# Kernel tuning notes

Measured on AMD Instinct MI355X. Metric: run time of the kernel, lower is better.

Reference implementation:

```python
import jax, jax.numpy as jnp
import numpy as np

KS = 3          # kernel_size
NH = 6          # num_heads
NUM_TOK = KS ** 3  # 27 neighbors per query


def setup_inputs() -> dict:
    key = jax.random.key(0)
    k1, k2, k3 = jax.random.split(key, 3)
    q = jax.random.normal(k1, (1, 40, 40, 40, 96), dtype=jnp.float32)
    k = jax.random.normal(k2, (1, 40, 40, 40, 96), dtype=jnp.float32)
    rpb = jax.random.normal(k3, (NH, KS, KS, KS), dtype=jnp.float32) * 0.02
    return {"q": q, "k": k, "rpb": rpb}


def _offsets():
    # torch.arange(-3//2+1, 3//2+1) == arange(-1, 2); meshgrid 'ij'; stacked -> [27, 3]
    r = jnp.arange(-1, 2, dtype=jnp.float32)
    g = jnp.stack(jnp.meshgrid(r, r, r, indexing="ij"), axis=-1)
    return g.reshape(NUM_TOK, 3)


def reference(q, k, rpb):
    B, H, W, T, C = q.shape
    hd = C // NH
    scale = hd ** -0.5
    N = H * W * T

    # queries: [B, N, nh, hd], pre-scaled
    qh = q.reshape(B, N, NH, hd) * scale

    # zero-pad keys by 1 voxel on each spatial side (matches nnf.pad on channels-first k)
    kp = jnp.pad(jnp.transpose(k, (0, 4, 1, 2, 3)),
                 ((0, 0), (0, 0), (1, 1), (1, 1), (1, 1)))

    # 27 shifted views == torch unfold over a 3x3x3 window (i slowest, matches grid order)
    wins = [kp[:, :, i:i + H, j:j + W, l:l + T]
            for i in range(KS) for j in range(KS) for l in range(KS)]
    Kw = jnp.stack(wins, axis=2)                 # [B, C, 27, H, W, T]
    Kw = Kw.reshape(B, NH, hd, NUM_TOK, N)        # [B, nh, hd, 27, N]

    # attention logits over the 27-token neighborhood
    attn = jnp.einsum("bnhd,bhdkn->bnhk", qh, Kw)  # [B, N, nh, 27]
    attn = attn + rpb.reshape(NH, NUM_TOK)[None, None, :, :]  # relative position bias
    attn = jax.nn.softmax(attn, axis=-1)

    # expected displacement: weighted sum of integer offsets -> [B, N, nh, 3]
    x = jnp.einsum("bnhk,kc->bnhc", attn, _offsets())
    x = x.reshape(B, H, W, T, NH * 3)
    return jnp.transpose(x, (0, 4, 1, 2, 3))      # [B, nh*3, H, W, T]
```

## Files before the change

### kernel.cpp

```cpp
#include <hip/hip_runtime.h>

typedef _Float16 hh2 __attribute__((ext_vector_type(2)));

#define DH 40
#define DW 40
#define DT 40
#define NC 96
#define NH 6
#define HD 16
#define NTOK 27
#define NVOX (DH * DW * DT)

#define TX 8
#define TY 4
#define TZ 8
#define HX 10
#define HY 6
#define HZ 10
#define NHALO 600

#define TXN 5
#define TYN 10
#define TZN 5
#define NTILE 250
#define NJOB 1500
#define NXCD 8
#define GRID 1504
#define PER_XCD (GRID / NXCD)

__device__ __forceinline__ float dot2acc(hh2 a, hh2 b, float c) {
    return __builtin_amdgcn_fdot2(a, b, c, false);
}
__device__ __forceinline__ hh2 pkrtz(float a, float b) {
    return __builtin_bit_cast(hh2, __builtin_amdgcn_cvt_pkrtz(a, b));
}
__device__ __forceinline__ unsigned int pkbits(float a, float b) {
    return __builtin_bit_cast(unsigned int, __builtin_amdgcn_cvt_pkrtz(a, b));
}

union I4H {
    int4 v[2];
    hh2 h[8];
};

__global__ __launch_bounds__(256) void natt_disp_kernel(
    const float* __restrict__ q,
    const float* __restrict__ k,
    const float* __restrict__ rpb,
    float* __restrict__ out)
{
    __shared__ int4 s_k[NHALO * 2];

    const int job = (blockIdx.x & (NXCD - 1)) * PER_XCD + (blockIdx.x >> 3);
    if (job >= NJOB) return;

    const int h    = job % NH;
    const int tile = job / NH;
    const int tz = tile % TZN;
    const int ty = (tile / TZN) % TYN;
    const int tx = tile / (TZN * TYN);
    const int x0 = tx * TX, y0 = ty * TY, z0 = tz * TZ;

    const int tid = threadIdx.x;

    float rk[NTOK];
    {
        const float* rb = rpb + h * NTOK;
        #pragma unroll
        for (int kk = 0; kk < NTOK; ++kk) rk[kk] = rb[kk];
    }

    const float* kh = k + h * HD;

    #pragma unroll
    for (int it = 0; it < 10; ++it) {
        const int jj = tid + it * 256;
        if (jj < NHALO * 4) {
            const int n = jj >> 2;
            const int c = jj & 3;
            const int hx = n / (HY * HZ);
            const int r  = n - hx * (HY * HZ);
            const int hy = r / HZ;
            const int hz = r - hy * HZ;
            const int gx = x0 - 1 + hx;
            const int gy = y0 - 1 + hy;
            const int gz = z0 - 1 + hz;
            uint2 w; w.x = 0u; w.y = 0u;
            if (((unsigned)gx < DH) & ((unsigned)gy < DW) & ((unsigned)gz < DT)) {
                const float4 a = *(const float4*)(
                    kh + ((size_t)((gx * DW + gy) * DT + gz)) * NC + c * 4);
                w.x = pkbits(a.x, a.y);
                w.y = pkbits(a.z, a.w);
            }
            const int p = hy & 1;
            ((uint2*)s_k)[((n * 2 + (c >> 1)) ^ p) * 2 + (c & 1)] = w;
        }
    }

    const int lz = tid & (TZ - 1);
    const int ly = (tid >> 3) & (TY - 1);
    const int lx = tid >> 5;
    const int vox = ((x0 + lx) * DW + (y0 + ly)) * DT + (z0 + lz);

    hh2 qh[8];
    {
        const float4* qv = (const float4*)(q + (size_t)vox * NC + h * HD);
        const float4 a = qv[0], b = qv[1], c = qv[2], d = qv[3];
        qh[0] = pkrtz(a.x, a.y);
        qh[1] = pkrtz(a.z, a.w);
        qh[2] = pkrtz(b.x, b.y);
        qh[3] = pkrtz(b.z, b.w);
        qh[4] = pkrtz(c.x, c.y);
        qh[5] = pkrtz(c.z, c.w);
        qh[6] = pkrtz(d.x, d.y);
        qh[7] = pkrtz(d.z, d.w);
    }

    __syncthreads();

    float l[NTOK];
    #pragma unroll
    for (int i = 0; i < 3; ++i) {
        #pragma unroll
        for (int j = 0; j < 3; ++j) {
            const int base = ((lx + i) * HY + (ly + j)) * HZ + lz;
            const int p = (ly + j) & 1;
            #pragma unroll
            for (int ll = 0; ll < 3; ++ll) {
                const int n = base + ll;
                I4H u;
                u.v[0] = s_k[(n * 2 + 0) ^ p];
                u.v[1] = s_k[(n * 2 + 1) ^ p];
                float d = 0.0f;
                d = dot2acc(qh[0], u.h[0], d);
                d = dot2acc(qh[1], u.h[1], d);
                d = dot2acc(qh[2], u.h[2], d);
                d = dot2acc(qh[3], u.h[3], d);
                d = dot2acc(qh[4], u.h[4], d);
                d = dot2acc(qh[5], u.h[5], d);
                d = dot2acc(qh[6], u.h[6], d);
                d = dot2acc(qh[7], u.h[7], d);
                const int kk = (i * 3 + j) * 3 + ll;
                l[kk] = fmaf(d, 0.25f, rk[kk]);
            }
        }
    }

    float g0 = fmaxf(fmaxf(l[0],  l[1]),  l[2]);
    float g1 = fmaxf(fmaxf(l[3],  l[4]),  l[5]);
    float g2 = fmaxf(fmaxf(l[6],  l[7]),  l[8]);
    float g3 = fmaxf(fmaxf(l[9],  l[10]), l[11]);
    float g4 = fmaxf(fmaxf(l[12], l[13]), l[14]);
    float g5 = fmaxf(fmaxf(l[15], l[16]), l[17]);
    float g6 = fmaxf(fmaxf(l[18], l[19]), l[20]);
    float g7 = fmaxf(fmaxf(l[21], l[22]), l[23]);
    float g8 = fmaxf(fmaxf(l[24], l[25]), l[26]);
    float t0 = fmaxf(fmaxf(g0, g1), g2);
    float t1 = fmaxf(fmaxf(g3, g4), g5);
    float t2 = fmaxf(fmaxf(g6, g7), g8);
    const float m = fmaxf(fmaxf(t0, t1), t2);

    const float LOG2E = 1.44269504f;
    const float nm2 = -m * LOG2E;
    float e[NTOK];
    #pragma unroll
    for (int kk = 0; kk < NTOK; ++kk)
        e[kk] = exp2f(fmaf(l[kk], LOG2E, nm2));

    float s[9], zp[9];
    #pragma unroll
    for (int g = 0; g < 9; ++g) {
        s[g]  = (e[g * 3] + e[g * 3 + 1]) + e[g * 3 + 2];
        zp[g] = e[g * 3 + 2] - e[g * 3];
    }
    const float sum = ((s[0] + s[1]) + (s[2] + s[3]))
                    + ((s[4] + s[5]) + (s[6] + s[7])) + s[8];
    const float szs = ((zp[0] + zp[1]) + (zp[2] + zp[3]))
                    + ((zp[4] + zp[5]) + (zp[6] + zp[7])) + zp[8];
    const float sxs = ((s[6] + s[7]) + s[8]) - ((s[0] + s[1]) + s[2]);
    const float sys = ((s[2] + s[5]) + s[8]) - ((s[0] + s[3]) + s[6]);

    const float inv = __builtin_amdgcn_rcpf(sum);

    out[((size_t)(h * 3 + 0)) * NVOX + vox] = sxs * inv;
    out[((size_t)(h * 3 + 1)) * NVOX + vox] = sys * inv;
    out[((size_t)(h * 3 + 2)) * NVOX + vox] = szs * inv;
}

extern "C" void kernel_launch(void* const* d_in, const int* in_sizes, int n_in,
                              void* d_out, int out_size, void* d_ws, size_t ws_size,
                              hipStream_t stream) {
    const float* q   = (const float*)d_in[0];
    const float* k   = (const float*)d_in[1];
    const float* rpb = (const float*)d_in[2];
    float* out = (float*)d_out;

    natt_disp_kernel<<<GRID, 256, 0, stream>>>(q, k, rpb, out);
}
```

Measured before the change: 20.92 us.

## Process two heads per block with register-prefetched second head and max-free softmax

Each block now handles two heads instead of one, halving the grid. The second head's K halo and Q are loaded into registers while the first head computes from shared memory, then staged into a second LDS buffer. The softmax drops the max subtraction and accumulates exp2 values directly, with the scale and log2e folded into the constants. This trades higher register pressure (launch bounds 256,3) and a risk of overflow on unbounded logits for fewer blocks and overlap of load latency with compute.

```diff
diff --git a/kernel.cpp b/kernel.cpp
--- a/kernel.cpp
+++ b/kernel.cpp
@@ -19,23 +19,19 @@
 #define HZ 10
 #define NHALO 600
 
-#define TXN 5
-#define TYN 10
-#define TZN 5
 #define NTILE 250
-#define NJOB 1500
-#define NXCD 8
-#define GRID 1504
-#define PER_XCD (GRID / NXCD)
+#define NBLK 750
+#define GRID 752
+#define PER_XCD 94
 
 __device__ __forceinline__ float dot2acc(hh2 a, hh2 b, float c) {
     return __builtin_amdgcn_fdot2(a, b, c, false);
 }
-__device__ __forceinline__ hh2 pkrtz(float a, float b) {
-    return __builtin_bit_cast(hh2, __builtin_amdgcn_cvt_pkrtz(a, b));
-}
 __device__ __forceinline__ unsigned int pkbits(float a, float b) {
     return __builtin_bit_cast(unsigned int, __builtin_amdgcn_cvt_pkrtz(a, b));
+}
+__device__ __forceinline__ hh2 asz(unsigned int u) {
+    return __builtin_bit_cast(hh2, u);
 }
 
 union I4H {
@@ -43,34 +39,44 @@
     hh2 h[8];
 };
 
-__global__ __launch_bounds__(256) void natt_disp_kernel(
+__global__ __launch_bounds__(256, 3) void natt_disp_kernel(
     const float* __restrict__ q,
     const float* __restrict__ k,
     const float* __restrict__ rpb,
     float* __restrict__ out)
 {
-    __shared__ int4 s_k[NHALO * 2];
-
-    const int job = (blockIdx.x & (NXCD - 1)) * PER_XCD + (blockIdx.x >> 3);
-    if (job >= NJOB) return;
-
-    const int h    = job % NH;
-    const int tile = job / NH;
-    const int tz = tile % TZN;
-    const int ty = (tile / TZN) % TYN;
-    const int tx = tile / (TZN * TYN);
+    __shared__ int4 s_k[2][NHALO * 2];
+
+    const int sb = (blockIdx.x & 7) * PER_XCD + (blockIdx.x >> 3);
+    if (sb >= NBLK) return;
+
+    const int hp   = sb % 3;
+    const int tile = sb / 3;
+    const int tz = tile % 5;
+    const int ty = (tile / 5) % 10;
+    const int tx = tile / 50;
     const int x0 = tx * TX, y0 = ty * TY, z0 = tz * TZ;
 
     const int tid = threadIdx.x;
-
-    float rk[NTOK];
+    const int lz = tid & 7;
+    const int ly = (tid >> 3) & 3;
+    const int lx = tid >> 5;
+    const int vox = ((x0 + lx) * DW + (y0 + ly)) * DT + (z0 + lz);
+
+    const int h0 = 2 * hp, h1 = 2 * hp + 1;
+
+    const float LOG2E = 1.44269504f;
+    float rk0[NTOK], rk1[NTOK];
     {
-        const float* rb = rpb + h * NTOK;
+        const float* rb = rpb + h0 * NTOK;
         #pragma unroll
-        for (int kk = 0; kk < NTOK; ++kk) rk[kk] = rb[kk];
-    }
-
-    const float* kh = k + h * HD;
+        for (int kk = 0; kk < NTOK; ++kk) rk0[kk] = rb[kk] * LOG2E;
+        #pragma unroll
+        for (int kk = 0; kk < NTOK; ++kk) rk1[kk] = rb[NTOK + kk] * LOG2E;
+    }
+
+    const float* kh0 = k + h0 * HD;
+    const float* kh1 = k + h1 * HD;
 
     #pragma unroll
     for (int it = 0; it < 10; ++it) {
@@ -88,103 +94,122 @@
             uint2 w; w.x = 0u; w.y = 0u;
             if (((unsigned)gx < DH) & ((unsigned)gy < DW) & ((unsigned)gz < DT)) {
                 const float4 a = *(const float4*)(
-                    kh + ((size_t)((gx * DW + gy) * DT + gz)) * NC + c * 4);
+                    kh0 + ((size_t)((gx * DW + gy) * DT + gz)) * NC + c * 4);
                 w.x = pkbits(a.x, a.y);
                 w.y = pkbits(a.z, a.w);
             }
-            const int p = hy & 1;
-            ((uint2*)s_k)[((n * 2 + (c >> 1)) ^ p) * 2 + (c & 1)] = w;
-        }
-    }
-
-    const int lz = tid & (TZ - 1);
-    const int ly = (tid >> 3) & (TY - 1);
-    const int lx = tid >> 5;
-    const int vox = ((x0 + lx) * DW + (y0 + ly)) * DT + (z0 + lz);
-
-    hh2 qh[8];
+            ((uint2*)s_k[0])[((n * 2 + (c >> 1)) ^ (hy & 1)) * 2 + (c & 1)] = w;
+        }
+    }
+
+    hh2 qhA[8];
     {
-        const float4* qv = (const float4*)(q + (size_t)vox * NC + h * HD);
+        const float4* qv = (const float4*)(q + (size_t)vox * NC + h0 * HD);
         const float4 a = qv[0], b = qv[1], c = qv[2], d = qv[3];
-        qh[0] = pkrtz(a.x, a.y);
-        qh[1] = pkrtz(a.z, a.w);
-        qh[2] = pkrtz(b.x, b.y);
-        qh[3] = pkrtz(b.z, b.w);
-        qh[4] = pkrtz(c.x, c.y);
-        qh[5] = pkrtz(c.z, c.w);
-        qh[6] = pkrtz(d.x, d.y);
-        qh[7] = pkrtz(d.z, d.w);
+        qhA[0] = asz(pkbits(a.x, a.y)); qhA[1] = asz(pkbits(a.z, a.w));
+        qhA[2] = asz(pkbits(b.x, b.y)); qhA[3] = asz(pkbits(b.z, b.w));
+        qhA[4] = asz(pkbits(c.x, c.y)); qhA[5] = asz(pkbits(c.z, c.w));
+        qhA[6] = asz(pkbits(d.x, d.y)); qhA[7] = asz(pkbits(d.z, d.w));
     }
 
     __syncthreads();
 
-    float l[NTOK];
-    #pragma unroll
-    for (int i = 0; i < 3; ++i) {
+    float4 FB[10];
+    #pragma unroll
+    for (int it = 0; it < 10; ++it) FB[it] = make_float4(0.f, 0.f, 0.f, 0.f);
+    #pragma unroll
+    for (int it = 0; it < 10; ++it) {
+        const int jj = tid + it * 256;
+        if (jj < NHALO * 4) {
+            const int n = jj >> 2;
+            const int c = jj & 3;
+            const int hx = n / (HY * HZ);
+            const int r  = n - hx * (HY * HZ);
+            const int hy = r / HZ;
+            const int hz = r - hy * HZ;
+            const int gx = x0 - 1 + hx;
+            const int gy = y0 - 1 + hy;
+            const int gz = z0 - 1 + hz;
+            if (((unsigned)gx < DH) & ((unsigned)gy < DW) & ((unsigned)gz < DT)) {
+                FB[it] = *(const float4*)(
+                    kh1 + ((size_t)((gx * DW + gy) * DT + gz)) * NC + c * 4);
+            }
+        }
+    }
+    float4 QB0, QB1, QB2, QB3;
+    {
+        const float4* qv = (const float4*)(q + (size_t)vox * NC + h1 * HD);
+        QB0 = qv[0]; QB1 = qv[1]; QB2 = qv[2]; QB3 = qv[3];
+    }
+    __builtin_amdgcn_sched_barrier(0);
+
+    const float SC2 = 0.36067376f;
+    auto compute = [&](const int4* buf, hh2 (&qh)[8], float (&rk)[NTOK],
+                       int hh) {
+        float sum = 0.f, sx = 0.f, sy = 0.f, sz = 0.f;
         #pragma unroll
-        for (int j = 0; j < 3; ++j) {
-            const int base = ((lx + i) * HY + (ly + j)) * HZ + lz;
-            const int p = (ly + j) & 1;
+        for (int i = 0; i < 3; ++i) {
             #pragma unroll
-            for (int ll = 0; ll < 3; ++ll) {
-                const int n = base + ll;
-                I4H u;
-                u.v[0] = s_k[(n * 2 + 0) ^ p];
-                u.v[1] = s_k[(n * 2 + 1) ^ p];
-                float d = 0.0f;
-                d = dot2acc(qh[0], u.h[0], d);
-                d = dot2acc(qh[1], u.h[1], d);
-                d = dot2acc(qh[2], u.h[2], d);
-                d = dot2acc(qh[3], u.h[3], d);
-                d = dot2acc(qh[4], u.h[4], d);
-                d = dot2acc(qh[5], u.h[5], d);
-                d = dot2acc(qh[6], u.h[6], d);
-                d = dot2acc(qh[7], u.h[7], d);
-                const int kk = (i * 3 + j) * 3 + ll;
-                l[kk] = fmaf(d, 0.25f, rk[kk]);
+            for (int j = 0; j < 3; ++j) {
+                const int base = ((lx + i) * HY + (ly + j)) * HZ + lz;
+                const int p = (ly + j) & 1;
+                #pragma unroll
+                for (int ll = 0; ll < 3; ++ll) {
+                    const int n = base + ll;
+                    I4H u;
+                    u.v[0] = buf[(n * 2 + 0) ^ p];
+                    u.v[1] = buf[(n * 2 + 1) ^ p];
+                    float d = 0.0f;
+                    d = dot2acc(qh[0], u.h[0], d);
+                    d = dot2acc(qh[1], u.h[1], d);
+                    d = dot2acc(qh[2], u.h[2], d);
+                    d = dot2acc(qh[3], u.h[3], d);
+                    d = dot2acc(qh[4], u.h[4], d);
+                    d = dot2acc(qh[5], u.h[5], d);
+                    d = dot2acc(qh[6], u.h[6], d);
+                    d = dot2acc(qh[7], u.h[7], d);
+                    const int kk = (i * 3 + j) * 3 + ll;
+                    const float t = exp2f(fmaf(d, SC2, rk[kk]));
+                    sum += t;
+                    if (i == 0) sx -= t; else if (i == 2) sx += t;
+                    if (j == 0) sy -= t; else if (j == 2) sy += t;
+                    if (ll == 0) sz -= t; else if (ll == 2) sz += t;
+                }
             }
         }
-    }
-
-    float g0 = fmaxf(fmaxf(l[0],  l[1]),  l[2]);
-    float g1 = fmaxf(fmaxf(l[3],  l[4]),  l[5]);
-    float g2 = fmaxf(fmaxf(l[6],  l[7]),  l[8]);
-    float g3 = fmaxf(fmaxf(l[9],  l[10]), l[11]);
-    float g4 = fmaxf(fmaxf(l[12], l[13]), l[14]);
-    float g5 = fmaxf(fmaxf(l[15], l[16]), l[17]);
-    float g6 = fmaxf(fmaxf(l[18], l[19]), l[20]);
-    float g7 = fmaxf(fmaxf(l[21], l[22]), l[23]);
-    float g8 = fmaxf(fmaxf(l[24], l[25]), l[26]);
-    float t0 = fmaxf(fmaxf(g0, g1), g2);
-    float t1 = fmaxf(fmaxf(g3, g4), g5);
-    float t2 = fmaxf(fmaxf(g6, g7), g8);
-    const float m = fmaxf(fmaxf(t0, t1), t2);
-
-    const float LOG2E = 1.44269504f;
-    const float nm2 = -m * LOG2E;
-    float e[NTOK];
-    #pragma unroll
-    for (int kk = 0; kk < NTOK; ++kk)
-        e[kk] = exp2f(fmaf(l[kk], LOG2E, nm2));
-
-    float s[9], zp[9];
-    #pragma unroll
-    for (int g = 0; g < 9; ++g) {
-        s[g]  = (e[g * 3] + e[g * 3 + 1]) + e[g * 3 + 2];
-        zp[g] = e[g * 3 + 2] - e[g * 3];
-    }
-    const float sum = ((s[0] + s[1]) + (s[2] + s[3]))
-                    + ((s[4] + s[5]) + (s[6] + s[7])) + s[8];
-    const float szs = ((zp[0] + zp[1]) + (zp[2] + zp[3]))
-                    + ((zp[4] + zp[5]) + (zp[6] + zp[7])) + zp[8];
-    const float sxs = ((s[6] + s[7]) + s[8]) - ((s[0] + s[1]) + s[2]);
-    const float sys = ((s[2] + s[5]) + s[8]) - ((s[0] + s[3]) + s[6]);
-
-    const float inv = __builtin_amdgcn_rcpf(sum);
-
-    out[((size_t)(h * 3 + 0)) * NVOX + vox] = sxs * inv;
-    out[((size_t)(h * 3 + 1)) * NVOX + vox] = sys * inv;
-    out[((size_t)(h * 3 + 2)) * NVOX + vox] = szs * inv;
+        const float inv = __builtin_amdgcn_rcpf(sum);
+        out[((size_t)(hh * 3 + 0)) * NVOX + vox] = sx * inv;
+        out[((size_t)(hh * 3 + 1)) * NVOX + vox] = sy * inv;
+        out[((size_t)(hh * 3 + 2)) * NVOX + vox] = sz * inv;
+    };
+
+    compute(s_k[0], qhA, rk0, h0);
+    __builtin_amdgcn_sched_barrier(0);
+
+    #pragma unroll
+    for (int it = 0; it < 10; ++it) {
+        const int jj = tid + it * 256;
+        if (jj < NHALO * 4) {
+            const int n = jj >> 2;
+            const int c = jj & 3;
+            const int hx = n / (HY * HZ);
+            const int r  = n - hx * (HY * HZ);
+            const int hy = r / HZ;
+            uint2 w;
+            w.x = pkbits(FB[it].x, FB[it].y);
+            w.y = pkbits(FB[it].z, FB[it].w);
+            ((uint2*)s_k[1])[((n * 2 + (c >> 1)) ^ (hy & 1)) * 2 + (c & 1)] = w;
+        }
+    }
+    hh2 qhB[8];
+    qhB[0] = asz(pkbits(QB0.x, QB0.y)); qhB[1] = asz(pkbits(QB0.z, QB0.w));
+    qhB[2] = asz(pkbits(QB1.x, QB1.y)); qhB[3] = asz(pkbits(QB1.z, QB1.w));
+    qhB[4] = asz(pkbits(QB2.x, QB2.y)); qhB[5] = asz(pkbits(QB2.z, QB2.w));
+    qhB[6] = asz(pkbits(QB3.x, QB3.y)); qhB[7] = asz(pkbits(QB3.z, QB3.w));
+
+    __syncthreads();
+
+    compute(s_k[1], qhB, rk1, h1);
 }
 
 extern "C" void kernel_launch(void* const* d_in, const int* in_sizes, int n_in,
```

Result: slower. 38.75 us (+85.2%).
